# Kernel tuning notes

Hardware: AMD Instinct MI355X
Metric: run time of the kernel (lower is better)

## Reference

```python
import jax, jax.numpy as jnp
import numpy as np

N_NODES = 100000   # n_user (70k) + m_item (30k)
N_EDGES = 2000000  # bidirectional user-item interaction edges
DIM = 64           # latent_dim = config['recdim']


def setup_inputs() -> dict:
    key = jax.random.key(0)
    k1, k2, k3, k4 = jax.random.split(key, 4)
    x = jax.random.normal(k1, (N_NODES, DIM), dtype=jnp.float32)
    edge_index = jax.random.randint(k2, (2, N_EDGES), 0, N_NODES, dtype=jnp.int32)
    # w_linears: Linear(2*D, D) per layer; stored as [in, out] so y = h @ W + b
    s = 1.0 / np.sqrt(2 * DIM)
    W0 = jax.random.normal(k3, (2 * DIM, DIM), dtype=jnp.float32) * s
    b0 = jnp.zeros((DIM,), dtype=jnp.float32)
    W1 = jax.random.normal(k4, (2 * DIM, DIM), dtype=jnp.float32) * s
    b1 = jnp.zeros((DIM,), dtype=jnp.float32)
    return {"x": x, "edge_index": edge_index, "W0": W0, "b0": b0, "W1": W1, "b1": b1}


def reference(x, edge_index, W0, b0, W1, b1):
    # SAGE-style: neighbor gather + mean aggregation + concat(self, agg) + per-layer linear
    n = x.shape[0]
    src = edge_index[0]  # message source nodes
    dst = edge_index[1]  # message destination nodes
    deg = jax.ops.segment_sum(jnp.ones(src.shape[0], x.dtype), dst, num_segments=n)
    inv_deg = (1.0 / jnp.maximum(deg, 1.0))[:, None]  # [N,1] mean normalizer

    h = x
    layers = ((W0, b0, True), (W1, b1, False))
    for W, b, apply_relu in layers:
        agg = jax.ops.segment_sum(h[src], dst, num_segments=n) * inv_deg  # [N,D] neighbor mean
        h = jnp.concatenate([h, agg], axis=1) @ W + b                      # [N,2D] @ [2D,D]
        if apply_relu:
            h = jax.nn.relu(h)
    return h
```

## Files before the change

### kernel.cpp

```cpp
#include <hip/hip_runtime.h>
#include <hip/hip_bf16.h>

#define N_NODES 100000
#define N_EDGES 2000000
#define DIM 64
#define NB 391
#define CAP 8192
#define PCAP 8192
#define EPB 4096
#define EPT 16
#define BIN_BLOCKS ((N_EDGES + EPB - 1) / EPB)
#define XCONV_BLOCKS (N_NODES * DIM / 4 / 256)

typedef __attribute__((ext_vector_type(8))) short short8;
typedef __attribute__((ext_vector_type(4))) float f32x4;
typedef __attribute__((ext_vector_type(2))) float f32x2;

__global__ __launch_bounds__(256) void binprep_kernel(const int* __restrict__ src,
                                                      const int* __restrict__ dst,
                                                      int* __restrict__ gbcur,
                                                      int* __restrict__ ebuf,
                                                      const float* __restrict__ x,
                                                      uint2* __restrict__ xb4,
                                                      int* __restrict__ xf8,
                                                      const float* __restrict__ W0,
                                                      const float* __restrict__ W1,
                                                      __hip_bfloat16* __restrict__ wfrag) {
    __shared__ int buf[EPB];
    __shared__ short bufb[EPB];
    __shared__ int a[512];
    __shared__ int lscan[NB], lcur[NB], gbase[NB];

    const int bid = blockIdx.x;
    if (bid >= BIN_BLOCKS) {
        const int pb = bid - BIN_BLOCKS;
        if (pb < XCONV_BLOCKS) {
            const int i = pb * 256 + threadIdx.x;
            const float4 v = ((const float4*)x)[i];
            __hip_bfloat162 p0 = __float22bfloat162_rn(make_float2(v.x, v.y));
            __hip_bfloat162 p1 = __float22bfloat162_rn(make_float2(v.z, v.w));
            uint2 ob;
            ob.x = *(unsigned int*)&p0;
            ob.y = *(unsigned int*)&p1;
            xb4[i] = ob;
            int w = __builtin_amdgcn_cvt_pk_fp8_f32(v.x, v.y, 0, false);
            w = __builtin_amdgcn_cvt_pk_fp8_f32(v.z, v.w, w, true);
            xf8[i] = w;
        } else {
            const int tid = (pb - XCONV_BLOCKS) * 256 + threadIdx.x;
            const int j    = tid & 7;
            const int lane = (tid >> 3) & 63;
            const int kc   = (tid >> 9) & 3;
            const int nt   = (tid >> 11) & 3;
            const int l    = tid >> 13;
            const int k = kc * 32 + (lane >> 4) * 8 + j;
            const int n = nt * 16 + (lane & 15);
            const float* W = l ? W1 : W0;
            wfrag[tid] = __float2bfloat16(W[k * 64 + n]);
        }
        return;
    }

    const int t = threadIdx.x;
    const int e0 = bid * EPB;
    const int cnt = min(EPB, N_EDGES - e0);

    for (int i = t; i < 512; i += 256) a[i] = 0;
    __syncthreads();

    int ls[EPT], ld[EPT];
    #pragma unroll
    for (int k = 0; k < EPT; ++k) {
        const int o = t + k * 256;
        if (o < cnt) {
            ls[k] = src[e0 + o];
            ld[k] = dst[e0 + o];
            atomicAdd(&a[ld[k] >> 8], 1);
        } else ld[k] = -1;
    }
    __syncthreads();

    #pragma unroll
    for (int d = 1; d < 512; d <<= 1) {
        const int idx = (t + 1) * 2 * d - 1;
        if (idx < 512) a[idx] += a[idx - d];
        __syncthreads();
    }
    if (t == 0) a[511] = 0;
    __syncthreads();
    #pragma unroll
    for (int d = 256; d >= 1; d >>= 1) {
        const int idx = (t + 1) * 2 * d - 1;
        if (idx < 512) {
            const int tmp = a[idx - d];
            a[idx - d] = a[idx];
            a[idx] += tmp;
        }
        __syncthreads();
    }
    for (int i = t; i < NB; i += 256) {
        const int c = a[i + 1] - a[i];
        lscan[i] = a[i];
        lcur[i]  = a[i];
        gbase[i] = c ? atomicAdd(&gbcur[i], c) : 0;
    }
    __syncthreads();

    #pragma unroll
    for (int k = 0; k < EPT; ++k) {
        if (ld[k] >= 0) {
            const int b = ld[k] >> 8;
            const int p = atomicAdd(&lcur[b], 1);
            buf[p]  = (ls[k] << 8) | (ld[k] & 255);
            bufb[p] = (short)b;
        }
    }
    __syncthreads();
    for (int i = t; i < cnt; i += 256) {
        const int pk = buf[i];
        const int b  = bufb[i];
        ebuf[b * CAP + gbase[b] + (i - lscan[b])] = pk;
    }
}

__global__ __launch_bounds__(256) void fillpass_kernel(const int* __restrict__ ebuf,
                                                       const int* __restrict__ gbcur,
                                                       int2* __restrict__ nodeinfo,
                                                       int* __restrict__ csr) {
    __shared__ int cnt[256];
    __shared__ int s[256];
    __shared__ int cur[256];
    const int b = blockIdx.x;
    const int t = threadIdx.x;
    const int nbase = b << 8;
    const int ecnt = gbcur[b];
    const int estart = b * CAP;

    cnt[t] = 0;
    __syncthreads();
    for (int i = t; i < ecnt; i += 256)
        atomicAdd(&cnt[ebuf[estart + i] & 255], 1);
    __syncthreads();

    const int deg  = cnt[t];
    const int pdeg = (deg + 3) & ~3;
    s[t] = pdeg;
    __syncthreads();
    #pragma unroll
    for (int off = 1; off < 256; off <<= 1) {
        int u = (t >= off) ? s[t - off] : 0;
        __syncthreads();
        s[t] += u;
        __syncthreads();
    }
    const int rp = b * PCAP + s[t] - pdeg;
    if (nbase + t < N_NODES) nodeinfo[nbase + t] = make_int2(rp, deg);
    cur[t] = rp;
    __syncthreads();

    for (int i = t; i < ecnt; i += 256) {
        const int pk = ebuf[estart + i];
        const int p = atomicAdd(&cur[pk & 255], 1);
        csr[p] = pk >> 8;
    }
    __syncthreads();
    for (int p = rp + deg; p < rp + pdeg; ++p)
        csr[p] = N_NODES;
}

__global__ __launch_bounds__(256) void gather_kernel(const uint2* __restrict__ f8tbl,
                                                     const int2* __restrict__ nodeinfo,
                                                     const uint4* __restrict__ csr4,
                                                     uint4* __restrict__ agg16) {
    const int g = threadIdx.x >> 3;
    const int r = threadIdx.x & 7;
    const int node = blockIdx.x * 32 + g;
    const int2 ni = nodeinfo[node];
    const int c0 = ni.x >> 2;
    const int deg = ni.y;
    const int rounds = (deg + 3) >> 2;

    float a0 = 0.f, a1 = 0.f, a2 = 0.f, a3 = 0.f;
    float a4 = 0.f, a5 = 0.f, a6 = 0.f, a7 = 0.f;

    #define CONSUME(u)                                                        \
        {                                                                     \
            f32x2 f01 = __builtin_amdgcn_cvt_pk_f32_fp8((u).x, false);        \
            f32x2 f23 = __builtin_amdgcn_cvt_pk_f32_fp8((u).x, true);         \
            f32x2 f45 = __builtin_amdgcn_cvt_pk_f32_fp8((u).y, false);        \
            f32x2 f67 = __builtin_amdgcn_cvt_pk_f32_fp8((u).y, true);         \
            a0 += f01.x; a1 += f01.y; a2 += f23.x; a3 += f23.y;               \
            a4 += f45.x; a5 += f45.y; a6 += f67.x; a7 += f67.y;               \
        }

    for (int t = 0; t < rounds; ++t) {
        const uint4 id = csr4[c0 + t];
        const uint2 u0 = f8tbl[(size_t)id.x * 8 + r];
        const uint2 u1 = f8tbl[(size_t)id.y * 8 + r];
        const uint2 u2 = f8tbl[(size_t)id.z * 8 + r];
        const uint2 u3 = f8tbl[(size_t)id.w * 8 + r];
        CONSUME(u0); CONSUME(u1); CONSUME(u2); CONSUME(u3);
    }
    #undef CONSUME

    const float inv = 1.0f / fmaxf((float)deg, 1.0f);
    __hip_bfloat162 p0 = __float22bfloat162_rn(make_float2(a0 * inv, a1 * inv));
    __hip_bfloat162 p1 = __float22bfloat162_rn(make_float2(a2 * inv, a3 * inv));
    __hip_bfloat162 p2 = __float22bfloat162_rn(make_float2(a4 * inv, a5 * inv));
    __hip_bfloat162 p3 = __float22bfloat162_rn(make_float2(a6 * inv, a7 * inv));
    uint4 ov;
    ov.x = *(unsigned int*)&p0;
    ov.y = *(unsigned int*)&p1;
    ov.z = *(unsigned int*)&p2;
    ov.w = *(unsigned int*)&p3;
    agg16[(size_t)node * 8 + r] = ov;
}

template <bool RELU, bool OUTF32, bool WRF8>
__global__ __launch_bounds__(256) void gemm_kernel(const unsigned short* __restrict__ hb,
                                                   const unsigned short* __restrict__ aggb,
                                                   const unsigned short* __restrict__ wfrag,
                                                   const float* __restrict__ bias,
                                                   float* __restrict__ outf,
                                                   unsigned short* __restrict__ outb,
                                                   unsigned char* __restrict__ outf8) {
    const int wave = threadIdx.x >> 6;
    const int lane = threadIdx.x & 63;
    const int m0 = (blockIdx.x * 4 + wave) * 16;
    const int quad = lane >> 4;
    const int lrow = lane & 15;
    const int m = min(m0 + lrow, N_NODES - 1);

    short8 bf[4][4];
    #pragma unroll
    for (int nt = 0; nt < 4; ++nt)
        #pragma unroll
        for (int kc = 0; kc < 4; ++kc)
            bf[nt][kc] = *(const short8*)(wfrag + (size_t)((nt * 4 + kc) * 64 + lane) * 8);

    f32x4 acc[4];
    #pragma unroll
    for (int nt = 0; nt < 4; ++nt) acc[nt] = f32x4{0.f, 0.f, 0.f, 0.f};

    #pragma unroll
    for (int kc = 0; kc < 4; ++kc) {
        const unsigned short* ap = (kc < 2)
            ? (hb   + (size_t)m * 64 + kc * 32 + quad * 8)
            : (aggb + (size_t)m * 64 + (kc - 2) * 32 + quad * 8);
        const short8 af = *(const short8*)ap;
        #pragma unroll
        for (int nt = 0; nt < 4; ++nt)
            acc[nt] = __builtin_amdgcn_mfma_f32_16x16x32_bf16(af, bf[nt][kc], acc[nt], 0, 0, 0);
    }

    #pragma unroll
    for (int nt = 0; nt < 4; ++nt) {
        const float bv = bias[nt * 16 + lrow];
        #pragma unroll
        for (int r = 0; r < 4; ++r) {
            const int mr = m0 + quad * 4 + r;
            if (mr < N_NODES) {
                float v = acc[nt][r] + bv;
                if (RELU) v = fmaxf(v, 0.f);
                const size_t off = (size_t)mr * 64 + nt * 16 + lrow;
                if (OUTF32) {
                    outf[off] = v;
                } else {
                    __hip_bfloat16 hv = __float2bfloat16(v);
                    outb[off] = *(unsigned short*)&hv;
                }
                if (WRF8) {
                    const int w8 = __builtin_amdgcn_cvt_pk_fp8_f32(v, v, 0, false);
                    outf8[off] = (unsigned char)(w8 & 0xff);
                }
            }
        }
    }
}

extern "C" void kernel_launch(void* const* d_in, const int* in_sizes, int n_in,
                              void* d_out, int out_size, void* d_ws, size_t ws_size,
                              hipStream_t stream) {
    const float* x  = (const float*)d_in[0];
    const int*   ei = (const int*)d_in[1];
    const float* W0 = (const float*)d_in[2];
    const float* b0 = (const float*)d_in[3];
    const float* W1 = (const float*)d_in[4];
    const float* b1 = (const float*)d_in[5];
    float* out = (float*)d_out;

    const int* src = ei;
    const int* dst = ei + N_EDGES;

    char* ws = (char*)d_ws;
    auto alloc = [&](size_t bytes) {
        char* p = ws;
        ws += (bytes + 255) & ~(size_t)255;
        return p;
    };
    int*  gbcur    = (int*)alloc((size_t)NB * 4);
    int2* nodeinfo = (int2*)alloc((size_t)N_NODES * 8);
    int*  ebuf     = (int*)alloc((size_t)NB * CAP * 4);
    int*  csr      = (int*)alloc((size_t)NB * PCAP * 4);
    unsigned short* xb   = (unsigned short*)alloc((size_t)N_NODES * DIM * 2);
    unsigned char*  xf8  = (unsigned char*)alloc((size_t)(N_NODES + 1) * DIM);
    unsigned short* aggb = (unsigned short*)alloc((size_t)N_NODES * DIM * 2);
    unsigned short* h1b  = (unsigned short*)alloc((size_t)N_NODES * DIM * 2);
    unsigned char*  h1f8 = (unsigned char*)alloc((size_t)(N_NODES + 1) * DIM);
    __hip_bfloat16* wfrag = (__hip_bfloat16*)alloc((size_t)2 * 8192 * 2);

    hipMemsetAsync(gbcur, 0, (size_t)NB * 4, stream);
    hipMemsetAsync(xf8  + (size_t)N_NODES * DIM, 0, DIM, stream);
    hipMemsetAsync(h1f8 + (size_t)N_NODES * DIM, 0, DIM, stream);

    binprep_kernel<<<BIN_BLOCKS + XCONV_BLOCKS + 64, 256, 0, stream>>>(
        src, dst, gbcur, ebuf, x, (uint2*)xb, (int*)xf8, W0, W1, wfrag);
    fillpass_kernel<<<NB, 256, 0, stream>>>(ebuf, gbcur, nodeinfo, csr);

    const int gemm_blocks = (N_NODES + 63) / 64;

    gather_kernel<<<N_NODES / 32, 256, 0, stream>>>((const uint2*)xf8, nodeinfo,
                                                    (const uint4*)csr, (uint4*)aggb);
    gemm_kernel<true, false, true><<<gemm_blocks, 256, 0, stream>>>(
        xb, aggb, (const unsigned short*)wfrag, b0, nullptr, h1b, h1f8);

    gather_kernel<<<N_NODES / 32, 256, 0, stream>>>((const uint2*)h1f8, nodeinfo,
                                                    (const uint4*)csr, (uint4*)aggb);
    gemm_kernel<false, true, false><<<gemm_blocks, 256, 0, stream>>>(
        h1b, aggb, (const unsigned short*)wfrag + 8192, b1, out, nullptr, nullptr);
}
```

Measured before the change: 209.1 us.

## Fuse neighbor gather with per-layer GEMM via shared-memory aggregate tile

Merges the gather and the GEMM kernels into one kernel per layer. Each block aggregates 64 nodes into a padded LDS tile, then feeds the MFMA GEMM straight from LDS. This removes the global bf16 aggregate buffer's write and read-back plus two launches. The zero sentinel rows are now written inside kernels instead of through separate memsets. The GEMM phase now waits behind the gather's irregular latency within each block, and the LDS use may lower occupancy.

```diff
diff --git a/kernel.cpp b/kernel.cpp
--- a/kernel.cpp
+++ b/kernel.cpp
@@ -11,6 +11,7 @@
 #define EPT 16
 #define BIN_BLOCKS ((N_EDGES + EPB - 1) / EPB)
 #define XCONV_BLOCKS (N_NODES * DIM / 4 / 256)
+#define LSTRIDE 144
 
 typedef __attribute__((ext_vector_type(8))) short short8;
 typedef __attribute__((ext_vector_type(4))) float f32x4;
@@ -46,6 +47,7 @@
             int w = __builtin_amdgcn_cvt_pk_fp8_f32(v.x, v.y, 0, false);
             w = __builtin_amdgcn_cvt_pk_fp8_f32(v.z, v.w, w, true);
             xf8[i] = w;
+            if (pb == 0 && threadIdx.x < 16) xf8[N_NODES * 16 + threadIdx.x] = 0;
         } else {
             const int tid = (pb - XCONV_BLOCKS) * 256 + threadIdx.x;
             const int j    = tid & 7;
@@ -168,113 +170,128 @@
         csr[p] = N_NODES;
 }
 
-__global__ __launch_bounds__(256) void gather_kernel(const uint2* __restrict__ f8tbl,
-                                                     const int2* __restrict__ nodeinfo,
-                                                     const uint4* __restrict__ csr4,
-                                                     uint4* __restrict__ agg16) {
-    const int g = threadIdx.x >> 3;
-    const int r = threadIdx.x & 7;
-    const int node = blockIdx.x * 32 + g;
-    const int2 ni = nodeinfo[node];
-    const int c0 = ni.x >> 2;
-    const int deg = ni.y;
-    const int rounds = (deg + 3) >> 2;
-
-    float a0 = 0.f, a1 = 0.f, a2 = 0.f, a3 = 0.f;
-    float a4 = 0.f, a5 = 0.f, a6 = 0.f, a7 = 0.f;
-
-    #define CONSUME(u)                                                        \
-        {                                                                     \
-            f32x2 f01 = __builtin_amdgcn_cvt_pk_f32_fp8((u).x, false);        \
-            f32x2 f23 = __builtin_amdgcn_cvt_pk_f32_fp8((u).x, true);         \
-            f32x2 f45 = __builtin_amdgcn_cvt_pk_f32_fp8((u).y, false);        \
-            f32x2 f67 = __builtin_amdgcn_cvt_pk_f32_fp8((u).y, true);         \
-            a0 += f01.x; a1 += f01.y; a2 += f23.x; a3 += f23.y;               \
-            a4 += f45.x; a5 += f45.y; a6 += f67.x; a7 += f67.y;               \
-        }
-
-    for (int t = 0; t < rounds; ++t) {
-        const uint4 id = csr4[c0 + t];
-        const uint2 u0 = f8tbl[(size_t)id.x * 8 + r];
-        const uint2 u1 = f8tbl[(size_t)id.y * 8 + r];
-        const uint2 u2 = f8tbl[(size_t)id.z * 8 + r];
-        const uint2 u3 = f8tbl[(size_t)id.w * 8 + r];
-        CONSUME(u0); CONSUME(u1); CONSUME(u2); CONSUME(u3);
-    }
-    #undef CONSUME
-
-    const float inv = 1.0f / fmaxf((float)deg, 1.0f);
-    __hip_bfloat162 p0 = __float22bfloat162_rn(make_float2(a0 * inv, a1 * inv));
-    __hip_bfloat162 p1 = __float22bfloat162_rn(make_float2(a2 * inv, a3 * inv));
-    __hip_bfloat162 p2 = __float22bfloat162_rn(make_float2(a4 * inv, a5 * inv));
-    __hip_bfloat162 p3 = __float22bfloat162_rn(make_float2(a6 * inv, a7 * inv));
-    uint4 ov;
-    ov.x = *(unsigned int*)&p0;
-    ov.y = *(unsigned int*)&p1;
-    ov.z = *(unsigned int*)&p2;
-    ov.w = *(unsigned int*)&p3;
-    agg16[(size_t)node * 8 + r] = ov;
-}
-
 template <bool RELU, bool OUTF32, bool WRF8>
-__global__ __launch_bounds__(256) void gemm_kernel(const unsigned short* __restrict__ hb,
-                                                   const unsigned short* __restrict__ aggb,
-                                                   const unsigned short* __restrict__ wfrag,
-                                                   const float* __restrict__ bias,
-                                                   float* __restrict__ outf,
-                                                   unsigned short* __restrict__ outb,
-                                                   unsigned char* __restrict__ outf8) {
-    const int wave = threadIdx.x >> 6;
-    const int lane = threadIdx.x & 63;
-    const int m0 = (blockIdx.x * 4 + wave) * 16;
-    const int quad = lane >> 4;
-    const int lrow = lane & 15;
-    const int m = min(m0 + lrow, N_NODES - 1);
-
-    short8 bf[4][4];
-    #pragma unroll
-    for (int nt = 0; nt < 4; ++nt)
-        #pragma unroll
-        for (int kc = 0; kc < 4; ++kc)
-            bf[nt][kc] = *(const short8*)(wfrag + (size_t)((nt * 4 + kc) * 64 + lane) * 8);
-
-    f32x4 acc[4];
-    #pragma unroll
-    for (int nt = 0; nt < 4; ++nt) acc[nt] = f32x4{0.f, 0.f, 0.f, 0.f};
-
-    #pragma unroll
-    for (int kc = 0; kc < 4; ++kc) {
-        const unsigned short* ap = (kc < 2)
-            ? (hb   + (size_t)m * 64 + kc * 32 + quad * 8)
-            : (aggb + (size_t)m * 64 + (kc - 2) * 32 + quad * 8);
-        const short8 af = *(const short8*)ap;
+__global__ __launch_bounds__(256) void sage_fused_kernel(
+        const uint2* __restrict__ f8tbl,
+        const unsigned short* __restrict__ hb,
+        const int2* __restrict__ nodeinfo,
+        const uint4* __restrict__ csr4,
+        const unsigned short* __restrict__ wfrag,
+        const float* __restrict__ bias,
+        float* __restrict__ outf,
+        unsigned short* __restrict__ outb,
+        unsigned char* __restrict__ outf8) {
+    __shared__ __align__(16) unsigned char aggL[64 * LSTRIDE];
+
+    const int tid = threadIdx.x;
+    const int base = blockIdx.x * 64;
+
+    {
+        const int g = tid >> 3;
+        const int r = tid & 7;
+
+        #define CONSUME(u, A)                                                 \
+            {                                                                 \
+                f32x2 f01 = __builtin_amdgcn_cvt_pk_f32_fp8((u).x, false);    \
+                f32x2 f23 = __builtin_amdgcn_cvt_pk_f32_fp8((u).x, true);     \
+                f32x2 f45 = __builtin_amdgcn_cvt_pk_f32_fp8((u).y, false);    \
+                f32x2 f67 = __builtin_amdgcn_cvt_pk_f32_fp8((u).y, true);     \
+                A[0] += f01.x; A[1] += f01.y; A[2] += f23.x; A[3] += f23.y;   \
+                A[4] += f45.x; A[5] += f45.y; A[6] += f67.x; A[7] += f67.y;   \
+            }
+
+        #pragma unroll
+        for (int half = 0; half < 2; ++half) {
+            const int ln = half * 32 + g;
+            const int node = base + ln;
+            int2 ni = (node < N_NODES) ? nodeinfo[node] : make_int2(0, 0);
+            const int c0 = ni.x >> 2;
+            const int deg = ni.y;
+            const int rounds = (deg + 3) >> 2;
+
+            float acc[8] = {0.f, 0.f, 0.f, 0.f, 0.f, 0.f, 0.f, 0.f};
+            for (int t = 0; t < rounds; ++t) {
+                const uint4 id = csr4[c0 + t];
+                const uint2 u0 = f8tbl[(size_t)id.x * 8 + r];
+                const uint2 u1 = f8tbl[(size_t)id.y * 8 + r];
+                const uint2 u2 = f8tbl[(size_t)id.z * 8 + r];
+                const uint2 u3 = f8tbl[(size_t)id.w * 8 + r];
+                CONSUME(u0, acc); CONSUME(u1, acc); CONSUME(u2, acc); CONSUME(u3, acc);
+            }
+            const float inv = 1.0f / fmaxf((float)deg, 1.0f);
+            __hip_bfloat162 p0 = __float22bfloat162_rn(make_float2(acc[0] * inv, acc[1] * inv));
+            __hip_bfloat162 p1 = __float22bfloat162_rn(make_float2(acc[2] * inv, acc[3] * inv));
+            __hip_bfloat162 p2 = __float22bfloat162_rn(make_float2(acc[4] * inv, acc[5] * inv));
+            __hip_bfloat162 p3 = __float22bfloat162_rn(make_float2(acc[6] * inv, acc[7] * inv));
+            uint4 ov;
+            ov.x = *(unsigned int*)&p0;
+            ov.y = *(unsigned int*)&p1;
+            ov.z = *(unsigned int*)&p2;
+            ov.w = *(unsigned int*)&p3;
+            *(uint4*)(aggL + ln * LSTRIDE + r * 16) = ov;
+        }
+        #undef CONSUME
+    }
+    __syncthreads();
+
+    {
+        const int wave = tid >> 6;
+        const int lane = tid & 63;
+        const int m0 = base + wave * 16;
+        const int quad = lane >> 4;
+        const int lrow = lane & 15;
+        const int m = min(m0 + lrow, N_NODES - 1);
+        const int ln = wave * 16 + lrow;
+
+        short8 bf[4][4];
         #pragma unroll
         for (int nt = 0; nt < 4; ++nt)
-            acc[nt] = __builtin_amdgcn_mfma_f32_16x16x32_bf16(af, bf[nt][kc], acc[nt], 0, 0, 0);
-    }
-
-    #pragma unroll
-    for (int nt = 0; nt < 4; ++nt) {
-        const float bv = bias[nt * 16 + lrow];
-        #pragma unroll
-        for (int r = 0; r < 4; ++r) {
-            const int mr = m0 + quad * 4 + r;
-            if (mr < N_NODES) {
-                float v = acc[nt][r] + bv;
-                if (RELU) v = fmaxf(v, 0.f);
-                const size_t off = (size_t)mr * 64 + nt * 16 + lrow;
-                if (OUTF32) {
-                    outf[off] = v;
-                } else {
-                    __hip_bfloat16 hv = __float2bfloat16(v);
-                    outb[off] = *(unsigned short*)&hv;
-                }
-                if (WRF8) {
-                    const int w8 = __builtin_amdgcn_cvt_pk_fp8_f32(v, v, 0, false);
-                    outf8[off] = (unsigned char)(w8 & 0xff);
+            #pragma unroll
+            for (int kc = 0; kc < 4; ++kc)
+                bf[nt][kc] = *(const short8*)(wfrag + (size_t)((nt * 4 + kc) * 64 + lane) * 8);
+
+        f32x4 acc[4];
+        #pragma unroll
+        for (int nt = 0; nt < 4; ++nt) acc[nt] = f32x4{0.f, 0.f, 0.f, 0.f};
+
+        #pragma unroll
+        for (int kc = 0; kc < 4; ++kc) {
+            short8 af;
+            if (kc < 2) {
+                af = *(const short8*)(hb + (size_t)m * 64 + kc * 32 + quad * 8);
+            } else {
+                af = *(const short8*)(aggL + ln * LSTRIDE + (kc - 2) * 64 + quad * 16);
+            }
+            #pragma unroll
+            for (int nt = 0; nt < 4; ++nt)
+                acc[nt] = __builtin_amdgcn_mfma_f32_16x16x32_bf16(af, bf[nt][kc], acc[nt], 0, 0, 0);
+        }
+
+        #pragma unroll
+        for (int nt = 0; nt < 4; ++nt) {
+            const float bv = bias[nt * 16 + lrow];
+            #pragma unroll
+            for (int r = 0; r < 4; ++r) {
+                const int mr = m0 + quad * 4 + r;
+                if (mr < N_NODES) {
+                    float v = acc[nt][r] + bv;
+                    if (RELU) v = fmaxf(v, 0.f);
+                    const size_t off = (size_t)mr * 64 + nt * 16 + lrow;
+                    if (OUTF32) {
+                        outf[off] = v;
+                    } else {
+                        __hip_bfloat16 hv = __float2bfloat16(v);
+                        outb[off] = *(unsigned short*)&hv;
+                    }
+                    if (WRF8) {
+                        const int w8 = __builtin_amdgcn_cvt_pk_fp8_f32(v, v, 0, false);
+                        outf8[off] = (unsigned char)(w8 & 0xff);
+                    }
                 }
             }
         }
+        if (WRF8 && blockIdx.x == 0 && tid < 8)
+            ((unsigned long long*)(outf8 + (size_t)N_NODES * DIM))[tid] = 0ULL;
     }
 }
 
@@ -304,28 +321,23 @@
     int*  csr      = (int*)alloc((size_t)NB * PCAP * 4);
     unsigned short* xb   = (unsigned short*)alloc((size_t)N_NODES * DIM * 2);
     unsigned char*  xf8  = (unsigned char*)alloc((size_t)(N_NODES + 1) * DIM);
-    unsigned short* aggb = (unsigned short*)alloc((size_t)N_NODES * DIM * 2);
     unsigned short* h1b  = (unsigned short*)alloc((size_t)N_NODES * DIM * 2);
     unsigned char*  h1f8 = (unsigned char*)alloc((size_t)(N_NODES + 1) * DIM);
     __hip_bfloat16* wfrag = (__hip_bfloat16*)alloc((size_t)2 * 8192 * 2);
 
     hipMemsetAsync(gbcur, 0, (size_t)NB * 4, stream);
-    hipMemsetAsync(xf8  + (size_t)N_NODES * DIM, 0, DIM, stream);
-    hipMemsetAsync(h1f8 + (size_t)N_NODES * DIM, 0, DIM, stream);
 
     binprep_kernel<<<BIN_BLOCKS + XCONV_BLOCKS + 64, 256, 0, stream>>>(
         src, dst, gbcur, ebuf, x, (uint2*)xb, (int*)xf8, W0, W1, wfrag);
     fillpass_kernel<<<NB, 256, 0, stream>>>(ebuf, gbcur, nodeinfo, csr);
 
-    const int gemm_blocks = (N_NODES + 63) / 64;
-
-    gather_kernel<<<N_NODES / 32, 256, 0, stream>>>((const uint2*)xf8, nodeinfo,
-                                                    (const uint4*)csr, (uint4*)aggb);
-    gemm_kernel<true, false, true><<<gemm_blocks, 256, 0, stream>>>(
-        xb, aggb, (const unsigned short*)wfrag, b0, nullptr, h1b, h1f8);
-
-    gather_kernel<<<N_NODES / 32, 256, 0, stream>>>((const uint2*)h1f8, nodeinfo,
-                                                    (const uint4*)csr, (uint4*)aggb);
-    gemm_kernel<false, true, false><<<gemm_blocks, 256, 0, stream>>>(
-        h1b, aggb, (const unsigned short*)wfrag + 8192, b1, out, nullptr, nullptr);
+    const int fused_blocks = (N_NODES + 63) / 64;
+
+    sage_fused_kernel<true, false, true><<<fused_blocks, 256, 0, stream>>>(
+        (const uint2*)xf8, xb, nodeinfo, (const uint4*)csr,
+        (const unsigned short*)wfrag, b0, nullptr, h1b, h1f8);
+
+    sage_fused_kernel<false, true, false><<<fused_blocks, 256, 0, stream>>>(
+        (const uint2*)h1f8, h1b, nodeinfo, (const uint4*)csr,
+        (const unsigned short*)wfrag + 8192, b1, out, nullptr, nullptr);
 }
```

Result: no change. 211.5 us (+1.1%).
